# Kernel tuning notes

Hardware: AMD Instinct MI355X
Metric: run time of the kernel (lower is better)

## Reference

```python
import jax, jax.numpy as jnp
import numpy as np

SHIFT, REDUCE = 0, 1
B, T, E, H = 128, 256, 300, 256


def _make_transitions(T, B):
    # Valid left-branching sequence: S, S, (R, S)*, ending with R -> 2T-1 steps.
    t = np.zeros(2 * T - 1, dtype=np.int32)
    t[2::2] = REDUCE
    return np.tile(t[:, None], (1, B))


def setup_inputs() -> dict:
    key = jax.random.key(0)
    ks = jax.random.split(key, 8)
    stdv = 1.0 / np.sqrt(H)
    u = lambda k, shape: jax.random.uniform(k, shape, jnp.float32, -stdv, stdv)
    return {
        "x": jax.random.normal(ks[0], (B, T, E), jnp.float32),
        "transitions": jnp.asarray(_make_transitions(T, B)),
        "Wp": u(ks[1], (E, H)),
        "bp": u(ks[2], (H,)),
        "Wg": u(ks[3], (E, H)),
        "bg": u(ks[4], (H,)),
        "Wr": u(ks[5], (2 * H, 5 * H)),
        "br": u(ks[6], (5 * H,)),
    }


def reference(x, transitions, Wp, bp, Wg, bg, Wr, br):
    Bb, Tt, _ = x.shape
    Hh = Wp.shape[1]
    # buffers: c = proj_x(x); h = sigmoid(proj_x_gate(x)) * tanh(c)
    c_buf = x @ Wp + bp                      # [B, T, H]
    h_buf = jax.nn.sigmoid(x @ Wg + bg) * jnp.tanh(c_buf)
    bidx = jnp.arange(Bb)

    stack_h0 = jnp.zeros((Bb, Tt, Hh), x.dtype)
    stack_c0 = jnp.zeros((Bb, Tt, Hh), x.dtype)
    sp0 = jnp.zeros((Bb,), jnp.int32)        # stack pointer
    bp0 = jnp.full((Bb,), Tt, jnp.int32)     # buffer pointer (pop from end)

    def step(carry, trans):
        sh, sc, sp, bptr = carry
        is_shift = trans == SHIFT            # [B] bool
        # SHIFT: pop last remaining buffer entry
        nbp = jnp.where(is_shift, bptr - 1, bptr)
        src = jnp.maximum(nbp, 0)
        sft_h = h_buf[bidx, src]
        sft_c = c_buf[bidx, src]
        # REDUCE: children = top two stack entries (r = top, l = below)
        ir = jnp.maximum(sp - 1, 0)
        il = jnp.maximum(sp - 2, 0)
        hl, cl = sh[bidx, il], sc[bidx, il]
        hr, cr = sh[bidx, ir], sc[bidx, ir]
        proj = jnp.concatenate([hl, hr], axis=-1) @ Wr + br   # [B, 5H]
        i, fl, fr, g, o = jnp.split(proj, 5, axis=-1)
        c_red = (jax.nn.sigmoid(fl) * cl + jax.nn.sigmoid(fr) * cr
                 + jax.nn.sigmoid(i) * jnp.tanh(g))
        h_red = jax.nn.sigmoid(o) * jnp.tanh(c_red)
        m = is_shift[:, None]
        h_new = jnp.where(m, sft_h, h_red)
        c_new = jnp.where(m, sft_c, c_red)
        pos = jnp.where(is_shift, sp, il)    # push location
        sh = sh.at[bidx, pos].set(h_new)
        sc = sc.at[bidx, pos].set(c_new)
        sp = jnp.where(is_shift, sp + 1, sp - 1)
        return (sh, sc, sp, nbp), None

    (sh, sc, sp, _), _ = jax.lax.scan(step, (stack_h0, stack_c0, sp0, bp0), transitions)
    # root h state = top of stack, h half only
    return sh[bidx, jnp.maximum(sp - 1, 0)]
```

## Files before the change

kernel.cpp:

```cpp
#include <hip/hip_runtime.h>
#include <hip/hip_fp16.h>
#include <math.h>

#define B_ 128
#define T_ 256
#define E_ 300
#define H_ 256
#define N5_ 1280
#define NSTEPS 511
#define DMAX 8

typedef _Float16 half8_t __attribute__((ext_vector_type(8)));
typedef float float4_t __attribute__((ext_vector_type(4)));
typedef int i4v __attribute__((ext_vector_type(4)));
typedef unsigned int u4v __attribute__((ext_vector_type(4)));

__device__ __forceinline__ float sigm_p(float x){ return 1.f/(1.f + expf(-x)); }
__device__ __forceinline__ float sigm(float x){ return __builtin_amdgcn_rcpf(1.f + __expf(-x)); }
__device__ __forceinline__ float ftanh(float x){
  float xc = fminf(15.f, fmaxf(-15.f, x));
  float e = __expf(-2.f*xc);
  return (1.f - e) * __builtin_amdgcn_rcpf(1.f + e);
}

__global__ __launch_bounds__(64) void k0a_scale(const float* __restrict__ Wr,
    float* __restrict__ scales){
  const int n = blockIdx.x, t = threadIdx.x;
  float m = 0.f;
  #pragma unroll
  for (int j=0;j<4;j++) m = fmaxf(m, fabsf(Wr[(size_t)(t+64*j)*N5_ + n]));
  #pragma unroll
  for (int off=32; off; off>>=1) m = fmaxf(m, __shfl_xor(m, off, 64));
  if (t==0) scales[n] = fmaxf(m, 1e-20f) * (1.f/127.f);
}

__global__ __launch_bounds__(256) void k0b_quant(const float* __restrict__ Wr,
    const float* __restrict__ scales, uint4* __restrict__ W4){
  int idx = blockIdx.x*256 + threadIdx.x;
  if (idx >= 20480) return;
  const int f    = idx >> 6;
  const int lane = idx & 63;
  const int w    = f / 80;
  const int r80  = f - w*80;
  const int g    = r80 >> 4;
  const int cg   = (r80 >> 2) & 3;
  const int kc   = r80 & 3;
  const int ml   = lane & 15, quad = lane >> 4;
  const int col  = g*256 + w*64 + cg*16 + ml;
  const float inv = 1.f / scales[col];
  unsigned int d[4];
  #pragma unroll
  for (int r=0; r<4; r++){
    unsigned int acc = 0;
    #pragma unroll
    for (int j=0; j<4; j++){
      const int k = kc*64 + quad*16 + r*4 + j;
      float wv = Wr[(size_t)k*N5_ + col];
      int q = (int)rintf(wv * inv);
      q = q > 127 ? 127 : (q < -127 ? -127 : q);
      acc |= ((unsigned int)(q & 255)) << (8*j);
    }
    d[r] = acc;
  }
  uint4 v; v.x=d[0]; v.y=d[1]; v.z=d[2]; v.w=d[3];
  W4[idx] = v;
}

__global__ __launch_bounds__(256) void k0d_wrt(const float* __restrict__ Wr,
    _Float16* __restrict__ Wr2t){
  int idx = blockIdx.x*256 + threadIdx.x;
  const int col = idx >> 8, k = idx & 255;
  Wr2t[(size_t)col*H_ + k] = (_Float16)Wr[(size_t)(256 + k)*N5_ + col];
}

__global__ __launch_bounds__(256) void k1_proj(
    const float* __restrict__ x, const float* __restrict__ Wp, const float* __restrict__ bp,
    const float* __restrict__ Wg, const float* __restrict__ bg,
    _Float16* __restrict__ h2, _Float16* __restrict__ c2){
  __shared__ __align__(16) _Float16 As [64*32];
  __shared__ __align__(16) _Float16 BsP[64*32];
  __shared__ __align__(16) _Float16 BsG[64*32];
  const int tid = threadIdx.x;
  const int row0 = blockIdx.x * 64;
  const int n0   = blockIdx.y * 64;
  const int wave = tid >> 6, lane = tid & 63;
  const int ml = lane & 15, quad = lane >> 4;
  float4_t accP[4], accG[4];
  #pragma unroll
  for (int i=0;i<4;i++){ accP[i]=(float4_t)(0.f); accG[i]=(float4_t)(0.f); }
  const int ar = tid >> 2, ak = (tid & 3) * 8;
  const int bk = tid >> 3, bn = (tid & 7) * 8;
  for (int kk = 0; kk < E_; kk += 32){
    __syncthreads();
    {
      const float* src = x + (size_t)(row0 + ar)*E_ + kk + ak;
      float v[8];
      #pragma unroll
      for (int q=0;q<2;q++){
        if (kk + ak + q*4 + 4 <= E_){
          float4_t f = *(const float4_t*)(src + q*4);
          v[q*4+0]=f.x; v[q*4+1]=f.y; v[q*4+2]=f.z; v[q*4+3]=f.w;
        } else {
          #pragma unroll
          for (int j=0;j<4;j++){ int kg = kk+ak+q*4+j; v[q*4+j] = (kg<E_) ? src[q*4+j] : 0.f; }
        }
      }
      #pragma unroll
      for (int j=0;j<8;j++) As[ar*32 + ak + j] = (_Float16)v[j];
    }
    {
      const int kg = kk + bk;
      if (kg < E_){
        const float* sp_ = Wp + (size_t)kg*H_ + n0 + bn;
        const float* sg_ = Wg + (size_t)kg*H_ + n0 + bn;
        float4_t p0 = *(const float4_t*)sp_, p1 = *(const float4_t*)(sp_+4);
        float4_t g0 = *(const float4_t*)sg_, g1 = *(const float4_t*)(sg_+4);
        float pv[8]={p0.x,p0.y,p0.z,p0.w,p1.x,p1.y,p1.z,p1.w};
        float gv[8]={g0.x,g0.y,g0.z,g0.w,g1.x,g1.y,g1.z,g1.w};
        #pragma unroll
        for (int j=0;j<8;j++){ BsP[(bn+j)*32+bk]=(_Float16)pv[j]; BsG[(bn+j)*32+bk]=(_Float16)gv[j]; }
      } else {
        #pragma unroll
        for (int j=0;j<8;j++){ BsP[(bn+j)*32+bk]=(_Float16)0.f; BsG[(bn+j)*32+bk]=(_Float16)0.f; }
      }
    }
    __syncthreads();
    half8_t a = *(const half8_t*)&As[(wave*16 + ml)*32 + quad*8];
    #pragma unroll
    for (int nt=0; nt<4; nt++){
      half8_t b1 = *(const half8_t*)&BsP[(nt*16 + ml)*32 + quad*8];
      accP[nt] = __builtin_amdgcn_mfma_f32_16x16x32_f16(a, b1, accP[nt], 0,0,0);
      half8_t b2 = *(const half8_t*)&BsG[(nt*16 + ml)*32 + quad*8];
      accG[nt] = __builtin_amdgcn_mfma_f32_16x16x32_f16(a, b2, accG[nt], 0,0,0);
    }
  }
  #pragma unroll
  for (int nt=0; nt<4; nt++){
    #pragma unroll
    for (int r=0;r<4;r++){
      int row = row0 + wave*16 + quad*4 + r;
      int col = n0 + nt*16 + ml;
      float c = accP[nt][r] + bp[col];
      float g = accG[nt][r] + bg[col];
      float h = sigm_p(g) * tanhf(c);
      size_t o = (size_t)row*H_ + col;
      c2[o] = (_Float16)c;
      h2[o] = (_Float16)h;
    }
  }
}

__global__ __launch_bounds__(256) void k2_rproj(
    const _Float16* __restrict__ h2, const _Float16* __restrict__ Wr2t,
    const float* __restrict__ br, _Float16* __restrict__ R2){
  __shared__ __align__(16) _Float16 As[128*32];
  __shared__ __align__(16) _Float16 Bs[128*32];
  const int tid = threadIdx.x;
  const int row0 = blockIdx.x*128, col0 = blockIdx.y*128;
  const int wave = tid>>6, lane = tid&63, ml = lane&15, quad = lane>>4;
  const int wr = wave>>1, wc = wave&1;

  float4_t acc[4][4];
  #pragma unroll
  for (int i=0;i<4;i++)
    #pragma unroll
    for (int j=0;j<4;j++) acc[i][j]=(float4_t)(0.f);

  for (int ks=0; ks<8; ks++){
    const int k0 = ks*32;
    __syncthreads();
    #pragma unroll
    for (int p=0; p<2; p++){
      const int flat = p*256 + tid;
      const int r  = flat >> 2;
      const int kq = (flat & 3) * 8;
      *(half8_t*)&As[r*32 + kq] = *(const half8_t*)(h2   + (size_t)(row0 + r)*H_ + k0 + kq);
      *(half8_t*)&Bs[r*32 + kq] = *(const half8_t*)(Wr2t + (size_t)(col0 + r)*H_ + k0 + kq);
    }
    __syncthreads();
    half8_t a[4], b[4];
    #pragma unroll
    for (int mi=0; mi<4; mi++) a[mi] = *(const half8_t*)&As[(wr*64 + mi*16 + ml)*32 + quad*8];
    #pragma unroll
    for (int ni=0; ni<4; ni++) b[ni] = *(const half8_t*)&Bs[(wc*64 + ni*16 + ml)*32 + quad*8];
    #pragma unroll
    for (int mi=0; mi<4; mi++)
      #pragma unroll
      for (int ni=0; ni<4; ni++)
        acc[mi][ni] = __builtin_amdgcn_mfma_f32_16x16x32_f16(a[mi], b[ni], acc[mi][ni], 0,0,0);
  }

  #pragma unroll
  for (int mi=0; mi<4; mi++)
    #pragma unroll
    for (int ni=0; ni<4; ni++)
      #pragma unroll
      for (int r=0; r<4; r++){
        const int row = row0 + wr*64 + mi*16 + quad*4 + r;
        const int col = col0 + wc*64 + ni*16 + ml;
        R2[(size_t)row*N5_ + col] = (_Float16)(acc[mi][ni][r] + br[col]);
      }
}

#define K3_LDS_BYTES 86016

#define DECL8(g) u4v bf##g##_0_0, bf##g##_0_1, bf##g##_0_2, bf##g##_0_3, \
                     bf##g##_1_0, bf##g##_1_1, bf##g##_1_2, bf##g##_1_3;
#define LOAD8(g) \
  bf##g##_0_0 = wb[((g)*16 + 0)*64]; bf##g##_0_1 = wb[((g)*16 + 1)*64]; \
  bf##g##_0_2 = wb[((g)*16 + 2)*64]; bf##g##_0_3 = wb[((g)*16 + 3)*64]; \
  bf##g##_1_0 = wb[((g)*16 + 4)*64]; bf##g##_1_1 = wb[((g)*16 + 5)*64]; \
  bf##g##_1_2 = wb[((g)*16 + 6)*64]; bf##g##_1_3 = wb[((g)*16 + 7)*64];

#define MFA(ACC, AF, BF) asm("v_mfma_i32_16x16x64_i8 %0, %1, %2, %0" \
    : "+v"(ACC) : "v"(AF), "a"(BF));
#define MFV(ACC, AF, BF) asm("v_mfma_i32_16x16x64_i8 %0, %1, %2, %0" \
    : "+v"(ACC) : "v"(AF), "v"(BF));
#define FENCE_IN2(A0,A1)  asm volatile("s_nop 1" : "+v"(A0), "+v"(A1));
#define FENCE_OUT2(A0,A1) asm volatile("s_nop 7\n\ts_nop 7" : "+v"(A0), "+v"(A1));
#define BARRIER() asm volatile("s_waitcnt lgkmcnt(0)\n\ts_barrier" ::: "memory")

#define GCHAIN2(g, DST) { \
  i4v A0={0,0,0,0}, A1={0,0,0,0}; \
  FENCE_IN2(A0,A1) \
  MFA(A0,af0,bf##g##_0_0) MFA(A1,af0,bf##g##_1_0) \
  MFA(A0,af1,bf##g##_0_1) MFA(A1,af1,bf##g##_1_1) \
  MFA(A0,af2,bf##g##_0_2) MFA(A1,af2,bf##g##_1_2) \
  MFA(A0,af3,bf##g##_0_3) MFA(A1,af3,bf##g##_1_3) \
  FENCE_OUT2(A0,A1) \
  DST = hsel ? A1.x : A0.x; }

#define GCHAIN2_G4(DST) { \
  const u4v og00=lwg4[0],   og01=lwg4[64],  og02=lwg4[128], og03=lwg4[192]; \
  const u4v og10=lwg4[256], og11=lwg4[320], og12=lwg4[384], og13=lwg4[448]; \
  i4v A0={0,0,0,0}, A1={0,0,0,0}; \
  FENCE_IN2(A0,A1) \
  MFV(A0,af0,og00) MFV(A1,af0,og10) \
  MFV(A0,af1,og01) MFV(A1,af1,og11) \
  MFV(A0,af2,og02) MFV(A1,af2,og12) \
  MFV(A0,af3,og03) MFV(A1,af3,og13) \
  FENCE_OUT2(A0,A1) \
  DST = hsel ? A1.x : A0.x; }

#define PAIR_STEP(IDX, RD, WR) { \
  BARRIER(); \
  float a0=(float)pA0, a1=(float)pA1, a2=(float)pA2, a3=(float)pA3, a4=(float)pA4; \
  const float tc = (float)pAc; \
  const u4v* sRD = (const u4v*)(sI8 + (RD)*H_); \
  const u4v af0 = sRD[quad], af1 = sRD[4+quad], af2 = sRD[8+quad], af3 = sRD[12+quad]; \
  { int rrow = 253-(IDX); if (rrow < 0) rrow = 0; \
    const _Float16* rr = R2 + ((size_t)b*T_ + rrow)*N5_ + col; \
    pA0=rr[0]; pA1=rr[256]; pA2=rr[512]; pA3=rr[768]; pA4=rr[1024]; \
    int crow = 252-(IDX); if (crow < 0) crow = 0; \
    pAc = c2[((size_t)b*T_ + crow)*H_ + col]; } \
  int d0,d1,d2,d3,d4; \
  GCHAIN2(0, d0)  a0 += scf0*(float)d0; \
  GCHAIN2(1, d1)  a1 += scf1*(float)d1; \
  GCHAIN2(2, d2)  a2 += scf2*(float)d2; \
  GCHAIN2(3, d3)  a3 += scf3*(float)d3; \
  GCHAIN2_G4(d4)  a4 += scf4*(float)d4; \
  const float cnew = sigm(a1)*cl + sigm(a2)*cr + sigm(a0)*ftanh(a3); \
  const float hnew = sigm(a4)*ftanh(cnew); \
  sI8[(WR)*H_ + col] = (char)(int)rintf(hnew*127.f); \
  cl = cnew; cr = tc; \
}

__global__ __launch_bounds__(512, 2) void k3_scan(
    const int* __restrict__ trans, const _Float16* __restrict__ h2, const _Float16* __restrict__ c2,
    const _Float16* __restrict__ R2, const uint4* __restrict__ W4,
    const float* __restrict__ scales, const float* __restrict__ Wr,
    const float* __restrict__ br, float* __restrict__ out){
  extern __shared__ char smem[];
  u4v*   wlds  = (u4v*)smem;
  float* sh_   = (float*)(smem + 65536);
  float* sc_   = (float*)(smem + 73728);
  char*  sI8   = (char*)(smem + 81920);
  const u4v* sI4 = (const u4v*)(smem + 81920);
  int* trs     = (int*)(smem + 83968);

  const int b = blockIdx.x, tid = threadIdx.x;
  const int lane = tid & 63, w8 = tid >> 6;
  const int quad = (lane >> 4) & 3;
  const int hsel = (lane >> 4) & 1;
  const int col  = (w8 << 5) + (lane & 31);
  const int w4   = w8 >> 1, cg0 = (w8 & 1) * 2;

  const u4v* WB4v = (const u4v*)W4;
  const u4v* wb   = WB4v + ((size_t)w4*80 + cg0*4)*64 + lane;

  DECL8(0) DECL8(1) DECL8(2) DECL8(3)
  LOAD8(0) LOAD8(1) LOAD8(2) LOAD8(3)

  #pragma unroll
  for (int t=0; t<8; t++){
    const int flat = t*512 + tid;
    const int fd   = flat >> 6;
    const int dl   = flat & 63;
    const int w8d  = fd >> 3;
    const int ii   = (fd >> 2) & 1;
    const int kc   = fd & 3;
    const int cg   = (w8d & 1)*2 + ii;
    const int srcf = (w8d >> 1)*80 + 4*16 + cg*4 + kc;
    wlds[flat] = WB4v[(size_t)srcf*64 + dl];
  }
  const u4v* lwg4 = wlds + (size_t)w8*512 + lane;

  const float scf0 = scales[col       ] * (1.f/127.f);
  const float scf1 = scales[col +  256] * (1.f/127.f);
  const float scf2 = scales[col +  512] * (1.f/127.f);
  const float scf3 = scales[col +  768] * (1.f/127.f);
  const float scf4 = scales[col + 1024] * (1.f/127.f);

  trs[tid] = (tid < NSTEPS) ? trans[(size_t)tid*B_ + b] : 1;
  for (int i = tid; i < DMAX*H_; i += 512){ sh_[i]=0.f; sc_[i]=0.f; sI8[i]=0; }

  int myok = 1;
  if (tid < NSTEPS){ int e = (tid>=2 && (tid&1)==0) ? 1 : 0; if (trs[tid]!=e) myok=0; }
  const int ok = __syncthreads_and(myok);

  if (ok){
    const size_t hb = (size_t)b*T_*H_;
    const _Float16 h255 = h2[hb + 255*H_ + col];
    float cl = (float)c2[hb + 255*H_ + col];
    float cr = (float)c2[hb + 254*H_ + col];
    _Float16 pA0,pA1,pA2,pA3,pA4,pAc;
    { const _Float16* rr = R2 + ((size_t)b*T_ + 254)*N5_ + col;
      pA0=rr[0]; pA1=rr[256]; pA2=rr[512]; pA3=rr[768]; pA4=rr[1024];
      pAc = c2[hb + 253*H_ + col]; }
    sI8[col] = (char)(int)rintf((float)h255 * 127.f);
    #pragma unroll 1
    for (int i=0; i<254; i+=2){
      PAIR_STEP(i,   0, 1)
      PAIR_STEP(i+1, 1, 0)
    }
    {
      BARRIER();
      float a0=(float)pA0, a1=(float)pA1, a2=(float)pA2, a3=(float)pA3, a4=(float)pA4;
      const u4v* sRD = (const u4v*)sI8;
      const u4v af0 = sRD[quad], af1 = sRD[4+quad], af2 = sRD[8+quad], af3 = sRD[12+quad];
      int d0,d1,d2,d3,d4;
      GCHAIN2(0, d0)  a0 += scf0*(float)d0;
      GCHAIN2(1, d1)  a1 += scf1*(float)d1;
      GCHAIN2(2, d2)  a2 += scf2*(float)d2;
      GCHAIN2(3, d3)  a3 += scf3*(float)d3;
      GCHAIN2_G4(d4)  a4 += scf4*(float)d4;
      const float cnew = sigm(a1)*cl + sigm(a2)*cr + sigm(a0)*ftanh(a3);
      const float hnew = sigm(a4)*ftanh(cnew);
      if (lane < 32) out[(size_t)b*H_ + col] = hnew;
    }
    return;
  }

  int sp = 0, bptr = T_, prev_src = -1;
  for (int step=0; step<NSTEPS; step++){
    __syncthreads();
    const int tr = trs[step];
    if (tr == 0){
      const int nbp = bptr - 1;
      const int src = nbp > 0 ? nbp : 0;
      const int slot = sp < 0 ? 0 : (sp > DMAX-1 ? DMAX-1 : sp);
      const size_t o = ((size_t)b*T_ + src)*H_ + col;
      const float wh = (float)h2[o], wc = (float)c2[o];
      sh_[slot*H_+col] = wh;
      sc_[slot*H_+col] = wc;
      sI8[slot*H_+col] = (char)(int)rintf(wh * 127.f);
      sp += 1; bptr = nbp; prev_src = src;
    } else {
      int ir = sp-1 > 0 ? sp-1 : 0;
      int il = sp-2 > 0 ? sp-2 : 0;
      ir = ir > DMAX-1 ? DMAX-1 : ir;
      il = il > DMAX-1 ? DMAX-1 : il;
      const int tg = prev_src;
      const float cl = sc_[il*H_+col];
      const float cr = sc_[ir*H_+col];
      const u4v af0 = sI4[il*16 +  0 + quad];
      const u4v af1 = sI4[il*16 +  4 + quad];
      const u4v af2 = sI4[il*16 +  8 + quad];
      const u4v af3 = sI4[il*16 + 12 + quad];
      float a0,a1,a2,a3,a4;
      if (tg >= 0){
        const _Float16* rr = R2 + ((size_t)b*T_ + tg)*N5_ + col;
        a0=(float)rr[0]; a1=(float)rr[256]; a2=(float)rr[512]; a3=(float)rr[768]; a4=(float)rr[1024];
      } else {
        a0=br[col]; a1=br[col+256]; a2=br[col+512]; a3=br[col+768]; a4=br[col+1024];
      }
      int d0,d1,d2,d3,d4;
      GCHAIN2(0, d0)  a0 += scf0*(float)d0;
      GCHAIN2(1, d1)  a1 += scf1*(float)d1;
      GCHAIN2(2, d2)  a2 += scf2*(float)d2;
      GCHAIN2(3, d3)  a3 += scf3*(float)d3;
      GCHAIN2_G4(d4)  a4 += scf4*(float)d4;
      if (tg < 0){
        for (int k=0; k<H_; k++){
          const float hrk = sh_[ir*H_+k];
          const float* wr = Wr + (size_t)(256+k)*N5_ + col;
          a0 += hrk*wr[0]; a1 += hrk*wr[256]; a2 += hrk*wr[512];
          a3 += hrk*wr[768]; a4 += hrk*wr[1024];
        }
      }
      const float cnew = sigm(a1)*cl + sigm(a2)*cr + sigm(a0)*ftanh(a3);
      const float hnew = sigm(a4)*ftanh(cnew);
      const int wq = (int)rintf(hnew * 127.f);
      __syncthreads();
      sh_[il*H_+col] = hnew;
      sc_[il*H_+col] = cnew;
      sI8[il*H_+col] = (char)wq;
      sp -= 1; prev_src = -1;
    }
  }
  __syncthreads();
  int fs = sp-1 > 0 ? sp-1 : 0;
  fs = fs > DMAX-1 ? DMAX-1 : fs;
  if (lane < 32) out[(size_t)b*H_ + col] = sh_[fs*H_+col];
}

extern "C" void kernel_launch(void* const* d_in, const int* in_sizes, int n_in,
                              void* d_out, int out_size, void* d_ws, size_t ws_size,
                              hipStream_t stream){
  const float* x    = (const float*)d_in[0];
  const int*   trn  = (const int*)  d_in[1];
  const float* Wp   = (const float*)d_in[2];
  const float* bp   = (const float*)d_in[3];
  const float* Wg   = (const float*)d_in[4];
  const float* bg   = (const float*)d_in[5];
  const float* Wr   = (const float*)d_in[6];
  const float* br   = (const float*)d_in[7];
  float* out = (float*)d_out;
  char* w = (char*)d_ws;
  _Float16* h2   = (_Float16*)(w);
  _Float16* c2   = (_Float16*)(w + (size_t)16777216);
  _Float16* R2   = (_Float16*)(w + (size_t)33554432);
  uint4*    W4   = (uint4*)   (w + (size_t)117440512);
  float*    scl  = (float*)   (w + (size_t)117768192);
  _Float16* Wr2t = (_Float16*)(w + (size_t)117773312);

  hipLaunchKernelGGL(k0a_scale, dim3(1280),     dim3(64),  0, stream, Wr, scl);
  hipLaunchKernelGGL(k0b_quant, dim3(80),       dim3(256), 0, stream, Wr, scl, W4);
  hipLaunchKernelGGL(k0d_wrt,   dim3(1280),     dim3(256), 0, stream, Wr, Wr2t);
  hipLaunchKernelGGL(k1_proj,   dim3(512, 4),   dim3(256), 0, stream, x, Wp, bp, Wg, bg, h2, c2);
  hipLaunchKernelGGL(k2_rproj,  dim3(256, 10),  dim3(256), 0, stream, h2, Wr2t, br, R2);
  hipLaunchKernelGGL(k3_scan,   dim3(128),      dim3(512), K3_LDS_BYTES, stream, trn, h2, c2, R2, W4, scl, Wr, br, out);
}
```

Before: 465.5 us.

## Pre-convert projection inputs to padded fp16 and enlarge k1 GEMM tiles

Adds two prep kernels: one converts x to fp16 padded to a K of 320, the other transposes Wp and Wg into fp16 column-major padded layouts. The input projection GEMM then loads aligned half8 vectors with no bounds checks or per-element conversion, and uses 128x128 tiles with a 4x4 MFMA grid per wave instead of 64x64, which raises reuse of each loaded operand. The cost is two extra launches and an extra pass over x through memory. The xt buffer shares workspace with R2, which is safe only because k2 overwrites R2 after k1 has consumed xt.

Result: slower. 482.4 us (+3.6%).

```diff
diff --git a/kernel.cpp b/kernel.cpp
--- a/kernel.cpp
+++ b/kernel.cpp
@@ -5,6 +5,7 @@
 #define B_ 128
 #define T_ 256
 #define E_ 300
+#define EP_ 320
 #define H_ 256
 #define N5_ 1280
 #define NSTEPS 511
@@ -73,81 +74,91 @@
   Wr2t[(size_t)col*H_ + k] = (_Float16)Wr[(size_t)(256 + k)*N5_ + col];
 }
 
+__global__ __launch_bounds__(256) void k0e_wpgt(const float* __restrict__ Wp,
+    const float* __restrict__ Wg, _Float16* __restrict__ Wpt,
+    _Float16* __restrict__ Wgt){
+  int idx = blockIdx.x*256 + threadIdx.x;
+  const int kp = idx >> 8, col = idx & 255;
+  const float* src = blockIdx.y ? Wg : Wp;
+  _Float16* dst = blockIdx.y ? Wgt : Wpt;
+  float v = (kp < E_) ? src[(size_t)kp*H_ + col] : 0.f;
+  dst[(size_t)col*EP_ + kp] = (_Float16)v;
+}
+
+__global__ __launch_bounds__(256) void k0x_xt(const float* __restrict__ x,
+    _Float16* __restrict__ xt){
+  int idx = blockIdx.x*256 + threadIdx.x;
+  const int row = idx / 40, kb = (idx - row*40)*8;
+  const float* src = x + (size_t)row*E_ + kb;
+  _Float16 v[8];
+  #pragma unroll
+  for (int j=0;j<8;j++){ int k=kb+j; v[j] = (_Float16)((k<E_) ? src[j] : 0.f); }
+  *(half8_t*)(xt + (size_t)row*EP_ + kb) = *(half8_t*)v;
+}
+
 __global__ __launch_bounds__(256) void k1_proj(
-    const float* __restrict__ x, const float* __restrict__ Wp, const float* __restrict__ bp,
-    const float* __restrict__ Wg, const float* __restrict__ bg,
+    const _Float16* __restrict__ xt, const _Float16* __restrict__ Wpt, const float* __restrict__ bp,
+    const _Float16* __restrict__ Wgt, const float* __restrict__ bg,
     _Float16* __restrict__ h2, _Float16* __restrict__ c2){
-  __shared__ __align__(16) _Float16 As [64*32];
-  __shared__ __align__(16) _Float16 BsP[64*32];
-  __shared__ __align__(16) _Float16 BsG[64*32];
+  __shared__ __align__(16) _Float16 As [128*32];
+  __shared__ __align__(16) _Float16 BsP[128*32];
+  __shared__ __align__(16) _Float16 BsG[128*32];
   const int tid = threadIdx.x;
-  const int row0 = blockIdx.x * 64;
-  const int n0   = blockIdx.y * 64;
-  const int wave = tid >> 6, lane = tid & 63;
-  const int ml = lane & 15, quad = lane >> 4;
-  float4_t accP[4], accG[4];
-  #pragma unroll
-  for (int i=0;i<4;i++){ accP[i]=(float4_t)(0.f); accG[i]=(float4_t)(0.f); }
-  const int ar = tid >> 2, ak = (tid & 3) * 8;
-  const int bk = tid >> 3, bn = (tid & 7) * 8;
-  for (int kk = 0; kk < E_; kk += 32){
+  const int row0 = blockIdx.x*128, col0 = blockIdx.y*128;
+  const int wave = tid>>6, lane = tid&63, ml = lane&15, quad = lane>>4;
+  const int wr = wave>>1, wc = wave&1;
+
+  float4_t accP[4][4], accG[4][4];
+  #pragma unroll
+  for (int i=0;i<4;i++)
+    #pragma unroll
+    for (int j=0;j<4;j++){ accP[i][j]=(float4_t)(0.f); accG[i][j]=(float4_t)(0.f); }
+
+  for (int ks=0; ks<10; ks++){
+    const int k0 = ks*32;
     __syncthreads();
-    {
-      const float* src = x + (size_t)(row0 + ar)*E_ + kk + ak;
-      float v[8];
+    #pragma unroll
+    for (int p=0; p<2; p++){
+      const int flat = p*256 + tid;
+      const int r  = flat >> 2;
+      const int kq = (flat & 3) * 8;
+      *(half8_t*)&As [r*32 + kq] = *(const half8_t*)(xt  + (size_t)(row0 + r)*EP_ + k0 + kq);
+      *(half8_t*)&BsP[r*32 + kq] = *(const half8_t*)(Wpt + (size_t)(col0 + r)*EP_ + k0 + kq);
+      *(half8_t*)&BsG[r*32 + kq] = *(const half8_t*)(Wgt + (size_t)(col0 + r)*EP_ + k0 + kq);
+    }
+    __syncthreads();
+    half8_t a[4], bpv[4], bgv[4];
+    #pragma unroll
+    for (int mi=0; mi<4; mi++) a[mi]   = *(const half8_t*)&As [(wr*64 + mi*16 + ml)*32 + quad*8];
+    #pragma unroll
+    for (int ni=0; ni<4; ni++){
+      bpv[ni] = *(const half8_t*)&BsP[(wc*64 + ni*16 + ml)*32 + quad*8];
+      bgv[ni] = *(const half8_t*)&BsG[(wc*64 + ni*16 + ml)*32 + quad*8];
+    }
+    #pragma unroll
+    for (int mi=0; mi<4; mi++)
       #pragma unroll
-      for (int q=0;q<2;q++){
-        if (kk + ak + q*4 + 4 <= E_){
-          float4_t f = *(const float4_t*)(src + q*4);
-          v[q*4+0]=f.x; v[q*4+1]=f.y; v[q*4+2]=f.z; v[q*4+3]=f.w;
-        } else {
-          #pragma unroll
-          for (int j=0;j<4;j++){ int kg = kk+ak+q*4+j; v[q*4+j] = (kg<E_) ? src[q*4+j] : 0.f; }
-        }
+      for (int ni=0; ni<4; ni++){
+        accP[mi][ni] = __builtin_amdgcn_mfma_f32_16x16x32_f16(a[mi], bpv[ni], accP[mi][ni], 0,0,0);
+        accG[mi][ni] = __builtin_amdgcn_mfma_f32_16x16x32_f16(a[mi], bgv[ni], accG[mi][ni], 0,0,0);
       }
+  }
+
+  #pragma unroll
+  for (int mi=0; mi<4; mi++)
+    #pragma unroll
+    for (int ni=0; ni<4; ni++)
       #pragma unroll
-      for (int j=0;j<8;j++) As[ar*32 + ak + j] = (_Float16)v[j];
-    }
-    {
-      const int kg = kk + bk;
-      if (kg < E_){
-        const float* sp_ = Wp + (size_t)kg*H_ + n0 + bn;
-        const float* sg_ = Wg + (size_t)kg*H_ + n0 + bn;
-        float4_t p0 = *(const float4_t*)sp_, p1 = *(const float4_t*)(sp_+4);
-        float4_t g0 = *(const float4_t*)sg_, g1 = *(const float4_t*)(sg_+4);
-        float pv[8]={p0.x,p0.y,p0.z,p0.w,p1.x,p1.y,p1.z,p1.w};
-        float gv[8]={g0.x,g0.y,g0.z,g0.w,g1.x,g1.y,g1.z,g1.w};
-        #pragma unroll
-        for (int j=0;j<8;j++){ BsP[(bn+j)*32+bk]=(_Float16)pv[j]; BsG[(bn+j)*32+bk]=(_Float16)gv[j]; }
-      } else {
-        #pragma unroll
-        for (int j=0;j<8;j++){ BsP[(bn+j)*32+bk]=(_Float16)0.f; BsG[(bn+j)*32+bk]=(_Float16)0.f; }
+      for (int r=0; r<4; r++){
+        const int row = row0 + wr*64 + mi*16 + quad*4 + r;
+        const int col = col0 + wc*64 + ni*16 + ml;
+        float c = accP[mi][ni][r] + bp[col];
+        float g = accG[mi][ni][r] + bg[col];
+        float h = sigm_p(g) * tanhf(c);
+        size_t o = (size_t)row*H_ + col;
+        c2[o] = (_Float16)c;
+        h2[o] = (_Float16)h;
       }
-    }
-    __syncthreads();
-    half8_t a = *(const half8_t*)&As[(wave*16 + ml)*32 + quad*8];
-    #pragma unroll
-    for (int nt=0; nt<4; nt++){
-      half8_t b1 = *(const half8_t*)&BsP[(nt*16 + ml)*32 + quad*8];
-      accP[nt] = __builtin_amdgcn_mfma_f32_16x16x32_f16(a, b1, accP[nt], 0,0,0);
-      half8_t b2 = *(const half8_t*)&BsG[(nt*16 + ml)*32 + quad*8];
-      accG[nt] = __builtin_amdgcn_mfma_f32_16x16x32_f16(a, b2, accG[nt], 0,0,0);
-    }
-  }
-  #pragma unroll
-  for (int nt=0; nt<4; nt++){
-    #pragma unroll
-    for (int r=0;r<4;r++){
-      int row = row0 + wave*16 + quad*4 + r;
-      int col = n0 + nt*16 + ml;
-      float c = accP[nt][r] + bp[col];
-      float g = accG[nt][r] + bg[col];
-      float h = sigm_p(g) * tanhf(c);
-      size_t o = (size_t)row*H_ + col;
-      c2[o] = (_Float16)c;
-      h2[o] = (_Float16)h;
-    }
-  }
 }
 
 __global__ __launch_bounds__(256) void k2_rproj(
@@ -430,14 +441,19 @@
   _Float16* h2   = (_Float16*)(w);
   _Float16* c2   = (_Float16*)(w + (size_t)16777216);
   _Float16* R2   = (_Float16*)(w + (size_t)33554432);
+  _Float16* xt   = (_Float16*)(w + (size_t)33554432);
   uint4*    W4   = (uint4*)   (w + (size_t)117440512);
   float*    scl  = (float*)   (w + (size_t)117768192);
   _Float16* Wr2t = (_Float16*)(w + (size_t)117773312);
+  _Float16* Wpt  = (_Float16*)(w + (size_t)118428672);
+  _Float16* Wgt  = (_Float16*)(w + (size_t)118592512);
 
   hipLaunchKernelGGL(k0a_scale, dim3(1280),     dim3(64),  0, stream, Wr, scl);
   hipLaunchKernelGGL(k0b_quant, dim3(80),       dim3(256), 0, stream, Wr, scl, W4);
   hipLaunchKernelGGL(k0d_wrt,   dim3(1280),     dim3(256), 0, stream, Wr, Wr2t);
-  hipLaunchKernelGGL(k1_proj,   dim3(512, 4),   dim3(256), 0, stream, x, Wp, bp, Wg, bg, h2, c2);
+  hipLaunchKernelGGL(k0e_wpgt,  dim3(320, 2),   dim3(256), 0, stream, Wp, Wg, Wpt, Wgt);
+  hipLaunchKernelGGL(k0x_xt,    dim3(5120),     dim3(256), 0, stream, x, xt);
+  hipLaunchKernelGGL(k1_proj,   dim3(256, 2),   dim3(256), 0, stream, xt, Wpt, bp, Wgt, bg, h2, c2);
   hipLaunchKernelGGL(k2_rproj,  dim3(256, 10),  dim3(256), 0, stream, h2, Wr2t, br, R2);
   hipLaunchKernelGGL(k3_scan,   dim3(128),      dim3(512), K3_LDS_BYTES, stream, trn, h2, c2, R2, W4, scl, Wr, br, out);
 }
```
